# Optimization experiments

Measured on AMD Instinct MI355X. Metric: run time of the kernel, lower is better.

Reference implementation:

```python
import jax, jax.numpy as jnp
import numpy as np

SEG_LENS = [2048, 8192]
DIL_RATES = [1, 2]


def _dilated_attention(q, k, v, is_causal):
    # q,k,v: [b, n, h, d]
    b, n, h, d = q.shape
    ng = len(SEG_LENS)
    g = h // ng  # heads per group (even split)
    scale = 1.0 / np.sqrt(d).astype(np.float32)
    out = jnp.zeros_like(q)
    for i, (s, r) in enumerate(zip(SEG_LENS, DIL_RATES)):
        hs = i * g
        offset = i % r  # offset_idx % dilation_rate, as in _create_dilation_pattern
        idx = np.arange(offset, s, r)  # dilated positions within a segment, length m
        m = idx.shape[0]
        ns = n // s  # number of segments
        # reshape to segments then gather dilated positions: [b, ns, m, g, d]
        qg = q[:, :, hs:hs + g, :].reshape(b, ns, s, g, d)[:, :, idx]
        kg = k[:, :, hs:hs + g, :].reshape(b, ns, s, g, d)[:, :, idx]
        vg = v[:, :, hs:hs + g, :].reshape(b, ns, s, g, d)[:, :, idx]
        # segment-local attention over dilated tokens only (structured sparsity)
        scores = jnp.einsum('bsqhd,bskhd->bshqk', qg, kg) * scale
        if is_causal:
            cm = np.tril(np.ones((m, m), dtype=bool))  # idx is sorted -> causal in dilated order
            scores = jnp.where(cm, scores, -jnp.inf)
        attn = jax.nn.softmax(scores, axis=-1)
        og = jnp.einsum('bshqk,bskhd->bsqhd', attn, vg)  # [b, ns, m, g, d]
        # scatter back to full segment positions; non-dilated positions stay zero
        full = jnp.zeros((b, ns, s, g, d), q.dtype).at[:, :, idx].set(og)
        out = out.at[:, :, hs:hs + g, :].set(full.reshape(b, n, g, d))
    return out


def setup_inputs() -> dict:
    key = jax.random.key(0)
    k1, k2, k3 = jax.random.split(key, 3)
    shape = (1, 8192, 8, 64)
    q = jax.random.normal(k1, shape, dtype=jnp.float32)
    k = jax.random.normal(k2, shape, dtype=jnp.float32)
    v = jax.random.normal(k3, shape, dtype=jnp.float32)
    return {"q": q, "k": k, "v": v, "is_causal": 1}


def reference(q, k, v, is_causal):
    return _dilated_attention(q, k, v, bool(is_causal))
```

## Files before the change

kernel.cpp:

```cpp
#include <hip/hip_runtime.h>


#define LP 72

typedef __attribute__((ext_vector_type(8))) short bf16x8;
typedef __attribute__((ext_vector_type(4))) float f32x4;
typedef const unsigned int __attribute__((address_space(1)))* gp1;
typedef unsigned int __attribute__((address_space(3)))* lp3;

__device__ __forceinline__ unsigned short f2bf(float f) {
  unsigned u = __builtin_bit_cast(unsigned, f);
  u += 0x7fff + ((u >> 16) & 1);
  return (unsigned short)(u >> 16);
}

__device__ __forceinline__ int region_base(int head) {
  return (head < 4) ? head * 524288 : 2097152 + (head - 4) * 262144;
}

__device__ __forceinline__ void gl_lds16(const unsigned short* g, unsigned short* l) {
  __builtin_amdgcn_global_load_lds((gp1)g, (lp3)l, 16, 0, 0);
}

__global__ __launch_bounds__(256, 4)
void prep_kernel(const float* __restrict__ K, const float* __restrict__ V,
                 unsigned short* __restrict__ Kb, unsigned short* __restrict__ Vt) {
  __shared__ unsigned short sT[64][LP];
  const int bid = blockIdx.x;
  int head, pos0, rate, off;
  if (bid < 512) { head = bid >> 7; pos0 = (bid & 127) * 64; rate = 1; off = 0; }
  else { int b = bid - 512; head = 4 + (b >> 6); pos0 = (b & 63) * 64; rate = 2; off = 1; }
  const int rb = region_base(head);
  const int tid = threadIdx.x;
  const int row = tid >> 2, dg = tid & 3;
  const long tok = (long)(pos0 + row) * rate + off;

  {
    const float* kp = K + tok * 512 + head * 64 + dg * 16;
    unsigned short tmp[16];
    #pragma unroll
    for (int i = 0; i < 4; ++i) {
      float4 f = ((const float4*)kp)[i];
      tmp[i * 4 + 0] = f2bf(f.x); tmp[i * 4 + 1] = f2bf(f.y);
      tmp[i * 4 + 2] = f2bf(f.z); tmp[i * 4 + 3] = f2bf(f.w);
    }
    const int s = row & 7;
    unsigned short* dstrow = Kb + rb + (long)(pos0 + row) * 64;
    *(int4*)(dstrow + (((2 * dg)     ^ s) * 8)) = ((int4*)tmp)[0];
    *(int4*)(dstrow + (((2 * dg + 1) ^ s) * 8)) = ((int4*)tmp)[1];
  }

  {
    const float* vp = V + tok * 512 + head * 64 + dg * 16;
    #pragma unroll
    for (int i = 0; i < 4; ++i) {
      float4 f = ((const float4*)vp)[i];
      unsigned* p = (unsigned*)&sT[row][dg * 16 + i * 4];
      p[0] = (unsigned)f2bf(f.x) | ((unsigned)f2bf(f.y) << 16);
      p[1] = (unsigned)f2bf(f.z) | ((unsigned)f2bf(f.w) << 16);
    }
  }
  __syncthreads();

  {
    const int wv = tid >> 6, lane = tid & 63;
    unsigned pk[8];
    #pragma unroll
    for (int j = 0; j < 8; ++j) {
      unsigned lo = sT[wv * 16 + 2 * j][lane];
      unsigned hi = sT[wv * 16 + 2 * j + 1][lane];
      pk[j] = lo | (hi << 16);
    }
    const int s = lane & 7;
    unsigned short* dstrow = Vt + rb + (long)pos0 * 64 + lane * 64;
    int4 a = {(int)pk[0], (int)pk[1], (int)pk[2], (int)pk[3]};
    int4 b = {(int)pk[4], (int)pk[5], (int)pk[6], (int)pk[7]};
    *(int4*)(dstrow + (((2 * wv)     ^ s) * 8)) = a;
    *(int4*)(dstrow + (((2 * wv + 1) ^ s) * 8)) = b;
  }
}

__global__ __launch_bounds__(256, 2)
void attn_kernel(const float* __restrict__ Q, const unsigned short* __restrict__ Kb,
                 const unsigned short* __restrict__ Vt, const int* __restrict__ IC,
                 float* __restrict__ O, float* __restrict__ Slots) {
  __shared__ __attribute__((aligned(16))) unsigned short sK[2][4096];
  __shared__ __attribute__((aligned(16))) unsigned short sV[2][4096];
  __shared__ __attribute__((aligned(16))) unsigned short sP[4][1024];

  const int bid = blockIdx.x;
  int head, q0, seg0, mseg, rate, off, grp, chunk, slot;
  if (bid < 512) {
    int h4 = bid & 3;
    int u = bid >> 2;
    chunk = u >> 6;
    int t = 63 - (u & 63);
    head = 4 + h4; seg0 = 0; mseg = 4096;
    rate = 2; off = 1; grp = 1;
    q0 = t * 64;
    slot = (h4 * 64 + t) * 2 + chunk;
  } else {
    int cc = bid - 512;
    int job = (cc & 7) | ((cc >> 8) << 3);
    int tloc = (cc & 255) >> 3;
    head = job & 3;
    seg0 = (job >> 2) * 2048;
    q0 = seg0 + tloc * 64; mseg = 2048;
    rate = 1; off = 0; grp = 0; chunk = 0; slot = 0;
  }
  const int rb = region_base(head);
  const bool causal = (*IC) != 0;
  const int tid = threadIdx.x, wave = tid >> 6, lane = tid & 63;
  const int l16 = lane & 15, quad = lane >> 4;
  const int ch0 = ((quad ^ (l16 & 7)) * 8);
  const int ch1 = ch0 ^ 32;

  const int qloc = q0 - seg0;
  const int diagkb = qloc >> 6;
  const int nkb = causal ? diagkb + 1 : (mseg >> 6);
  const int klo = grp ? chunk * 32 : 0;
  const int khi = grp ? min(nkb, klo + 32) : nkb;
  if (klo >= khi) return;

  const float QSCALE = 0.18033688011112042f;
  bf16x8 bQ[2];
  {
    long tok = (long)(q0 + wave * 16 + l16) * rate + off;
    const float* qp = Q + tok * 512 + head * 64 + quad * 8;
    #pragma unroll
    for (int kc = 0; kc < 2; ++kc) {
      float4 f0 = ((const float4*)(qp + kc * 32))[0];
      float4 f1 = ((const float4*)(qp + kc * 32))[1];
      bf16x8 a;
      a[0] = (short)f2bf(f0.x * QSCALE); a[1] = (short)f2bf(f0.y * QSCALE);
      a[2] = (short)f2bf(f0.z * QSCALE); a[3] = (short)f2bf(f0.w * QSCALE);
      a[4] = (short)f2bf(f1.x * QSCALE); a[5] = (short)f2bf(f1.y * QSCALE);
      a[6] = (short)f2bf(f1.z * QSCALE); a[7] = (short)f2bf(f1.w * QSCALE);
      bQ[kc] = a;
    }
  }

  f32x4 oacc[4];
  float lsum = 0.f;
  #pragma unroll
  for (int dt = 0; dt < 4; ++dt) oacc[dt] = (f32x4){0.f, 0.f, 0.f, 0.f};

  unsigned short* myP = &sP[wave][0];
  const unsigned short* Ksrc = Kb + rb + (long)seg0 * 64;
  const unsigned short* Vsrc = Vt + rb + (long)seg0 * 64;

  const int o0 = wave * 1024;
  const int lo = lane * 8;
  {
    const unsigned short* kt = Ksrc + (long)klo * 4096;
    const unsigned short* vt = Vsrc + (long)klo * 4096;
    gl_lds16(kt + o0 + lo,       &sK[0][o0]);
    gl_lds16(kt + o0 + 512 + lo, &sK[0][o0 + 512]);
    gl_lds16(vt + o0 + lo,       &sV[0][o0]);
    gl_lds16(vt + o0 + 512 + lo, &sV[0][o0 + 512]);
  }

  for (int kb = klo; kb < khi; ++kb) {
    const int cur = (kb - klo) & 1;
    __syncthreads();
    if (kb + 1 < khi) {
      const unsigned short* kt = Ksrc + (long)(kb + 1) * 4096;
      const unsigned short* vt = Vsrc + (long)(kb + 1) * 4096;
      gl_lds16(kt + o0 + lo,       &sK[cur ^ 1][o0]);
      gl_lds16(kt + o0 + 512 + lo, &sK[cur ^ 1][o0 + 512]);
      gl_lds16(vt + o0 + lo,       &sV[cur ^ 1][o0]);
      gl_lds16(vt + o0 + 512 + lo, &sV[cur ^ 1][o0 + 512]);
    }
    const unsigned short* kbuf = &sK[cur][0];
    const unsigned short* vbuf = &sV[cur][0];

    f32x4 sc[4];
    #pragma unroll
    for (int c = 0; c < 4; ++c) {
      const unsigned short* krow = &kbuf[(c * 16 + l16) * 64];
      bf16x8 a0 = *(const bf16x8*)(krow + ch0);
      bf16x8 a1 = *(const bf16x8*)(krow + ch1);
      f32x4 z = (f32x4){0.f, 0.f, 0.f, 0.f};
      z = __builtin_amdgcn_mfma_f32_16x16x32_bf16(a0, bQ[0], z, 0, 0, 0);
      z = __builtin_amdgcn_mfma_f32_16x16x32_bf16(a1, bQ[1], z, 0, 0, 0);
      sc[c] = z;
    }

    const bool needMask = causal && (kb == diagkb);
    const int myq = qloc + wave * 16 + l16;
    const int sw = l16 & 7;
    #pragma unroll
    for (int c = 0; c < 4; ++c) {
      unsigned short pb[4];
      #pragma unroll
      for (int r = 0; r < 4; ++r) {
        float e = __builtin_amdgcn_exp2f(sc[c][r]);
        if (needMask && (kb * 64 + c * 16 + quad * 4 + r > myq)) e = 0.f;
        lsum += e;
        pb[r] = f2bf(e);
      }
      unsigned w0 = (unsigned)pb[0] | ((unsigned)pb[1] << 16);
      unsigned w1 = (unsigned)pb[2] | ((unsigned)pb[3] << 16);
      const int wch = (c * 2 + (quad >> 1)) ^ sw;
      *(uint2*)&myP[l16 * 64 + wch * 8 + (quad & 1) * 4] = (uint2){w0, w1};
    }
    bf16x8 bP0 = *(const bf16x8*)&myP[l16 * 64 + ((quad ^ sw) << 3)];
    bf16x8 bP1 = *(const bf16x8*)&myP[l16 * 64 + (((4 + quad) ^ sw) << 3)];

    #pragma unroll
    for (int dt = 0; dt < 4; ++dt) {
      const unsigned short* vrow = &vbuf[(dt * 16 + l16) * 64];
      bf16x8 v0 = *(const bf16x8*)(vrow + ch0);
      bf16x8 v1 = *(const bf16x8*)(vrow + ch1);
      oacc[dt] = __builtin_amdgcn_mfma_f32_16x16x32_bf16(v0, bP0, oacc[dt], 0, 0, 0);
      oacc[dt] = __builtin_amdgcn_mfma_f32_16x16x32_bf16(v1, bP1, oacc[dt], 0, 0, 0);
    }
  }

  lsum += __shfl_xor(lsum, 16);
  lsum += __shfl_xor(lsum, 32);

  const int row = wave * 16 + l16;

  if (grp == 1) {
    float* S = Slots + (long)slot * 4160;
    #pragma unroll
    for (int dt = 0; dt < 4; ++dt)
      *(float4*)&S[row * 64 + dt * 16 + quad * 4] =
          (float4){oacc[dt][0], oacc[dt][1], oacc[dt][2], oacc[dt][3]};
    if (quad == 0) S[4096 + row] = lsum;
  } else {
    long tok = (long)(q0 + row) * rate + off;
    float inv = 1.0f / lsum;
    float* dst = O + tok * 512 + head * 64 + quad * 4;
    #pragma unroll
    for (int dt = 0; dt < 4; ++dt) {
      float4 v = {oacc[dt][0] * inv, oacc[dt][1] * inv,
                  oacc[dt][2] * inv, oacc[dt][3] * inv};
      *(float4*)(dst + dt * 16) = v;
    }
  }
}

__global__ __launch_bounds__(256, 4)
void combine_kernel(const float* __restrict__ Slots, const int* __restrict__ IC,
                    float* __restrict__ O) {
  const int b = blockIdx.x;
  const int h4 = b >> 6, t = b & 63;
  const bool causal = (*IC) != 0;
  const int nkb = causal ? t + 1 : 64;
  const int nc = (nkb > 32) ? 2 : 1;
  const float* s0 = Slots + (long)((h4 * 64 + t) * 2) * 4160;
  const int tid = threadIdx.x;
  const int row = tid >> 2, dq = (tid & 3) * 16;

  float4 acc[4];
  const float4* p0 = (const float4*)(s0 + row * 64 + dq);
  #pragma unroll
  for (int i = 0; i < 4; ++i) acc[i] = p0[i];
  float l = s0[4096 + row];
  if (nc == 2) {
    const float* s1 = s0 + 4160;
    const float4* p1 = (const float4*)(s1 + row * 64 + dq);
    #pragma unroll
    for (int i = 0; i < 4; ++i) {
      float4 v = p1[i];
      acc[i].x += v.x; acc[i].y += v.y; acc[i].z += v.z; acc[i].w += v.w;
    }
    l += s1[4096 + row];
  }
  const float inv = 1.0f / l;
  const long tok = (long)(t * 64 + row) * 2 + 1;
  float* dst = O + tok * 512 + (4 + h4) * 64 + dq;
  #pragma unroll
  for (int i = 0; i < 4; ++i) {
    float4 o = {acc[i].x * inv, acc[i].y * inv, acc[i].z * inv, acc[i].w * inv};
    ((float4*)dst)[i] = o;
  }
  float* dste = O + (tok - 1) * 512 + (4 + h4) * 64 + dq;
  const float4 z = {0.f, 0.f, 0.f, 0.f};
  #pragma unroll
  for (int i = 0; i < 4; ++i) ((float4*)dste)[i] = z;
}

extern "C" void kernel_launch(void* const* d_in, const int* in_sizes, int n_in,
                              void* d_out, int out_size, void* d_ws, size_t ws_size,
                              hipStream_t stream) {
  const float* q = (const float*)d_in[0];
  const float* k = (const float*)d_in[1];
  const float* v = (const float*)d_in[2];
  const int* ic = (const int*)d_in[3];
  unsigned short* Kb = (unsigned short*)d_ws;
  unsigned short* Vt = Kb + 3145728;
  float* Slots = (float*)((char*)d_ws + 12582912);
  prep_kernel<<<dim3(768), dim3(256), 0, stream>>>(k, v, Kb, Vt);
  attn_kernel<<<dim3(1024), dim3(256), 0, stream>>>(q, Kb, Vt, ic, (float*)d_out, Slots);
  combine_kernel<<<dim3(256), dim3(256), 0, stream>>>(Slots, ic, (float*)d_out);
}
```

Before: 139.7 us.

## Balance causal attention work with variable split-K chunks per query tile

Query tiles are now split into a number of key-block chunks that grows with their causal length, for the rate-2 heads and, newly, for the rate-1 heads too. Heavy tiles are scheduled first, which evens out per-block work and shortens the tail of the grid. Partial outputs are stored as bf16 instead of fp32 to halve slot traffic, and unsplit rate-2 tiles zero their even rows inside the attention kernel. This adds more blocks and a larger combine pass, and rounding partial sums to bf16 costs accuracy.

```diff
diff --git a/kernel.cpp b/kernel.cpp
--- a/kernel.cpp
+++ b/kernel.cpp
@@ -14,12 +14,20 @@
   return (unsigned short)(u >> 16);
 }
 
+__device__ __forceinline__ float bf2f(unsigned short u) {
+  return __builtin_bit_cast(float, ((unsigned)u) << 16);
+}
+
 __device__ __forceinline__ int region_base(int head) {
   return (head < 4) ? head * 524288 : 2097152 + (head - 4) * 262144;
 }
 
 __device__ __forceinline__ void gl_lds16(const unsigned short* g, unsigned short* l) {
   __builtin_amdgcn_global_load_lds((gp1)g, (lp3)l, 16, 0, 0);
+}
+
+__device__ __forceinline__ int g1_slot_off(int t) {
+  return (t < 32) ? 2 * (t - 16) : ((t < 48) ? 32 + 3 * (t - 32) : 80 + 4 * (t - 48));
 }
 
 __global__ __launch_bounds__(256, 4)
@@ -83,33 +91,41 @@
 __global__ __launch_bounds__(256, 2)
 void attn_kernel(const float* __restrict__ Q, const unsigned short* __restrict__ Kb,
                  const unsigned short* __restrict__ Vt, const int* __restrict__ IC,
-                 float* __restrict__ O, float* __restrict__ Slots) {
+                 float* __restrict__ O, char* __restrict__ SlotsB) {
   __shared__ __attribute__((aligned(16))) unsigned short sK[2][4096];
   __shared__ __attribute__((aligned(16))) unsigned short sV[2][4096];
   __shared__ __attribute__((aligned(16))) unsigned short sP[4][1024];
 
+  const bool causal = (*IC) != 0;
   const int bid = blockIdx.x;
-  int head, q0, seg0, mseg, rate, off, grp, chunk, slot;
-  if (bid < 512) {
-    int h4 = bid & 3;
-    int u = bid >> 2;
-    chunk = u >> 6;
-    int t = 63 - (u & 63);
-    head = 4 + h4; seg0 = 0; mseg = 4096;
-    rate = 2; off = 1; grp = 1;
+  int head, q0, seg0, rate, off, grp, nkb, nch, j, slot;
+  if (bid < 640) {
+    int h = bid & 3;
+    int m = 159 - (bid >> 2);
+    int t;
+    if (m < 16)      { t = m; j = 0; }
+    else if (m < 48) { int r = m - 16; t = 16 + (r >> 1); j = r & 1; }
+    else if (m < 96) { int r = m - 48; t = 32 + r / 3;    j = r % 3; }
+    else             { int r = m - 96; t = 48 + (r >> 2); j = r & 3; }
+    head = 4 + h; seg0 = 0; rate = 2; off = 1; grp = 1;
     q0 = t * 64;
-    slot = (h4 * 64 + t) * 2 + chunk;
+    nkb = causal ? t + 1 : 64;
+    nch = (t >> 4) + 1;
+    slot = (nch > 1) ? (h * 144 + g1_slot_off(t) + j) : -1;
   } else {
-    int cc = bid - 512;
-    int job = (cc & 7) | ((cc >> 8) << 3);
-    int tloc = (cc & 255) >> 3;
-    head = job & 3;
-    seg0 = (job >> 2) * 2048;
-    q0 = seg0 + tloc * 64; mseg = 2048;
-    rate = 1; off = 0; grp = 0; chunk = 0; slot = 0;
+    int b2 = bid - 640;
+    int J = b2 & 15;
+    int m = 47 - (b2 >> 4);
+    int u;
+    if (m < 16) { u = m; j = 0; }
+    else        { int r = m - 16; u = 16 + (r >> 1); j = r & 1; }
+    head = J & 3; seg0 = (J >> 2) * 2048; rate = 1; off = 0; grp = 0;
+    q0 = seg0 + u * 64;
+    nkb = causal ? u + 1 : 32;
+    nch = (u >> 4) + 1;
+    slot = (nch > 1) ? (576 + J * 32 + 2 * (u - 16) + j) : -1;
   }
   const int rb = region_base(head);
-  const bool causal = (*IC) != 0;
   const int tid = threadIdx.x, wave = tid >> 6, lane = tid & 63;
   const int l16 = lane & 15, quad = lane >> 4;
   const int ch0 = ((quad ^ (l16 & 7)) * 8);
@@ -117,9 +133,8 @@
 
   const int qloc = q0 - seg0;
   const int diagkb = qloc >> 6;
-  const int nkb = causal ? diagkb + 1 : (mseg >> 6);
-  const int klo = grp ? chunk * 32 : 0;
-  const int khi = grp ? min(nkb, klo + 32) : nkb;
+  const int klo = j * nkb / nch;
+  const int khi = (j + 1) * nkb / nch;
   if (klo >= khi) return;
 
   const float QSCALE = 0.18033688011112042f;
@@ -222,13 +237,16 @@
 
   const int row = wave * 16 + l16;
 
-  if (grp == 1) {
-    float* S = Slots + (long)slot * 4160;
-    #pragma unroll
-    for (int dt = 0; dt < 4; ++dt)
-      *(float4*)&S[row * 64 + dt * 16 + quad * 4] =
-          (float4){oacc[dt][0], oacc[dt][1], oacc[dt][2], oacc[dt][3]};
-    if (quad == 0) S[4096 + row] = lsum;
+  if (slot >= 0) {
+    unsigned short* Sp = (unsigned short*)(SlotsB + (long)slot * 8448);
+    #pragma unroll
+    for (int dt = 0; dt < 4; ++dt) {
+      ushort4 pk = {f2bf(oacc[dt][0]), f2bf(oacc[dt][1]),
+                    f2bf(oacc[dt][2]), f2bf(oacc[dt][3])};
+      *(ushort4*)&Sp[row * 64 + dt * 16 + quad * 4] = pk;
+    }
+    if (quad == 0)
+      ((float*)(SlotsB + (long)slot * 8448 + 8192))[row] = lsum;
   } else {
     long tok = (long)(q0 + row) * rate + off;
     float inv = 1.0f / lsum;
@@ -239,48 +257,66 @@
                   oacc[dt][2] * inv, oacc[dt][3] * inv};
       *(float4*)(dst + dt * 16) = v;
     }
+    if (grp == 1) {
+      int p = q0 + (tid >> 2);
+      int dd = (tid & 3) * 16;
+      float4 z4 = {0.f, 0.f, 0.f, 0.f};
+      float4* dste = (float4*)(O + (long)(2 * p) * 512 + head * 64 + dd);
+      dste[0] = z4; dste[1] = z4; dste[2] = z4; dste[3] = z4;
+    }
   }
 }
 
 __global__ __launch_bounds__(256, 4)
-void combine_kernel(const float* __restrict__ Slots, const int* __restrict__ IC,
+void combine_kernel(const char* __restrict__ SlotsB, const int* __restrict__ IC,
                     float* __restrict__ O) {
   const int b = blockIdx.x;
-  const int h4 = b >> 6, t = b & 63;
-  const bool causal = (*IC) != 0;
-  const int nkb = causal ? t + 1 : 64;
-  const int nc = (nkb > 32) ? 2 : 1;
-  const float* s0 = Slots + (long)((h4 * 64 + t) * 2) * 4160;
   const int tid = threadIdx.x;
-  const int row = tid >> 2, dq = (tid & 3) * 16;
-
-  float4 acc[4];
-  const float4* p0 = (const float4*)(s0 + row * 64 + dq);
+  const int row = tid >> 2, d0 = (tid & 3) * 16;
+  int head, nch, slotbase, q0, rate, offt;
+  bool evens;
+  if (b < 192) {
+    int h = b / 48, t = 16 + (b % 48);
+    nch = (t >> 4) + 1;
+    slotbase = h * 144 + g1_slot_off(t);
+    head = 4 + h; q0 = t * 64; rate = 2; offt = 1; evens = true;
+  } else {
+    int b2 = b - 192;
+    int J = b2 >> 4, u = 16 + (b2 & 15);
+    nch = 2;
+    slotbase = 576 + J * 32 + 2 * (u - 16);
+    head = J & 3; q0 = (J >> 2) * 2048 + u * 64; rate = 1; offt = 0; evens = false;
+  }
+
+  float acc[16];
   #pragma unroll
-  for (int i = 0; i < 4; ++i) acc[i] = p0[i];
-  float l = s0[4096 + row];
-  if (nc == 2) {
-    const float* s1 = s0 + 4160;
-    const float4* p1 = (const float4*)(s1 + row * 64 + dq);
-    #pragma unroll
-    for (int i = 0; i < 4; ++i) {
-      float4 v = p1[i];
-      acc[i].x += v.x; acc[i].y += v.y; acc[i].z += v.z; acc[i].w += v.w;
-    }
-    l += s1[4096 + row];
+  for (int i = 0; i < 16; ++i) acc[i] = 0.f;
+  float l = 0.f;
+  for (int c = 0; c < nch; ++c) {
+    const unsigned short* Sp = (const unsigned short*)(SlotsB + (long)(slotbase + c) * 8448);
+    #pragma unroll
+    for (int k = 0; k < 4; ++k) {
+      ushort4 v = *(const ushort4*)&Sp[row * 64 + d0 + k * 4];
+      acc[k * 4 + 0] += bf2f(v.x); acc[k * 4 + 1] += bf2f(v.y);
+      acc[k * 4 + 2] += bf2f(v.z); acc[k * 4 + 3] += bf2f(v.w);
+    }
+    l += ((const float*)(SlotsB + (long)(slotbase + c) * 8448 + 8192))[row];
   }
   const float inv = 1.0f / l;
-  const long tok = (long)(t * 64 + row) * 2 + 1;
-  float* dst = O + tok * 512 + (4 + h4) * 64 + dq;
+  const long tok = (long)(q0 + row) * rate + offt;
+  float* dst = O + tok * 512 + head * 64 + d0;
   #pragma unroll
-  for (int i = 0; i < 4; ++i) {
-    float4 o = {acc[i].x * inv, acc[i].y * inv, acc[i].z * inv, acc[i].w * inv};
-    ((float4*)dst)[i] = o;
-  }
-  float* dste = O + (tok - 1) * 512 + (4 + h4) * 64 + dq;
-  const float4 z = {0.f, 0.f, 0.f, 0.f};
-  #pragma unroll
-  for (int i = 0; i < 4; ++i) ((float4*)dste)[i] = z;
+  for (int k = 0; k < 4; ++k) {
+    float4 o = {acc[k * 4 + 0] * inv, acc[k * 4 + 1] * inv,
+                acc[k * 4 + 2] * inv, acc[k * 4 + 3] * inv};
+    ((float4*)dst)[k] = o;
+  }
+  if (evens) {
+    float* dste = O + (tok - 1) * 512 + head * 64 + d0;
+    const float4 z = {0.f, 0.f, 0.f, 0.f};
+    #pragma unroll
+    for (int k = 0; k < 4; ++k) ((float4*)dste)[k] = z;
+  }
 }
 
 extern "C" void kernel_launch(void* const* d_in, const int* in_sizes, int n_in,
@@ -292,8 +328,8 @@
   const int* ic = (const int*)d_in[3];
   unsigned short* Kb = (unsigned short*)d_ws;
   unsigned short* Vt = Kb + 3145728;
-  float* Slots = (float*)((char*)d_ws + 12582912);
+  char* SlotsB = (char*)d_ws + 12582912;
   prep_kernel<<<dim3(768), dim3(256), 0, stream>>>(k, v, Kb, Vt);
-  attn_kernel<<<dim3(1024), dim3(256), 0, stream>>>(q, Kb, Vt, ic, (float*)d_out, Slots);
-  combine_kernel<<<dim3(256), dim3(256), 0, stream>>>(Slots, ic, (float*)d_out);
-}
+  attn_kernel<<<dim3(1408), dim3(256), 0, stream>>>(q, Kb, Vt, ic, (float*)d_out, SlotsB);
+  combine_kernel<<<dim3(448), dim3(256), 0, stream>>>(SlotsB, ic, (float*)d_out);
+}
```

After: 141.3 us. Within noise of the previous version (+1.2%).
